# Performance work log

Measured on AMD Instinct MI355X. Metric: run time of the kernel, lower is better.

The kernel has to match this reference:

```python
import jax, jax.numpy as jnp
import numpy as np


def setup_inputs() -> dict:
    key = jax.random.key(0)
    k1, k2, k3 = jax.random.split(key, 3)
    T, B, C, H, W = 8, 4, 128, 96, 96
    h = w = 384  # original visibility-map resolution
    values = jax.random.normal(k1, (T + 1, B, C, H, W), jnp.float32)
    tvmap = jax.random.uniform(k2, (B, 1, h, w), jnp.float32)
    rvmaps = jax.random.uniform(k3, (T, B, 1, h, w), jnp.float32)
    return {"values": values, "tvmap": tvmap, "rvmaps": rvmaps}


def _resize_bin(m, H, W):
    # bilinear resize (half-pixel centers == torch align_corners=False), then > 0.5 threshold
    r = jax.image.resize(m, m.shape[:-2] + (H, W), method="bilinear")
    return (r > 0.5).astype(m.dtype)


def reference(values, tvmap, rvmaps):
    t_feat = values[0]          # [B,C,H,W]
    r_feats = values[1:]        # [T,B,C,H,W]
    T, B, C, H, W = r_feats.shape

    tv = _resize_bin(tvmap, H, W)                           # [B,1,H,W]
    rv = jax.vmap(lambda m: _resize_bin(m, H, W))(rvmaps)   # [T,B,1,H,W]
    vmap_ = tv[None] * rv                                   # [T,B,1,H,W]

    # per-frame masked similarity score gs
    gs = jnp.sum(vmap_ * t_feat[None] * r_feats, axis=(-1, -2, -3))  # [T,B]
    v_sum = jnp.sum(vmap_[:, :, 0], axis=(-1, -2))                   # [T,B]
    empty = v_sum < 1e-4
    gs = jnp.where(empty, 0.0, gs) / (v_sum + empty.astype(gs.dtype)) / C

    gss = gs.transpose(1, 0)[:, None, :, None, None]   # [B,1,T,1,1]
    vmaps = rv.transpose(1, 2, 0, 3, 4)                # [B,1,T,H,W]

    # masked softmax over frame axis (dim=2) with zero-guard
    mv = gss * vmaps
    mx = jnp.max(mv, axis=2, keepdims=True)
    me = jnp.exp(mv - mx) * vmaps
    ms = jnp.sum(me, axis=2, keepdims=True)
    ms = ms + (ms < 1e-4).astype(ms.dtype)
    c_match = jax.lax.stop_gradient(me / ms)           # [B,1,T,H,W]

    rf = r_feats.transpose(1, 2, 0, 3, 4)              # [B,C,T,H,W]
    c_out = jnp.sum(rf * c_match, axis=2)              # [B,C,H,W]

    c_mask = jnp.sum(c_match * vmaps, axis=2)          # [B,1,H,W]
    c_mask = jax.lax.stop_gradient(1.0 - jnp.mean(c_mask, axis=1, keepdims=True))

    out = jnp.concatenate([t_feat, c_out, c_mask], axis=1)  # [B, 2C+1, H, W]
    return out, c_mask, gs
```

## Files before the change

kernel.cpp:

```cpp
#include <hip/hip_runtime.h>
#include <math.h>

#define T_ 8
#define B_ 4
#define C_ 128
#define HW_ 9216
#define IN_HW_ 147456

typedef float nat_f4 __attribute__((ext_vector_type(4)));

__device__ static const double d_wm[8]  = {0.03125, 0.09375, 0.15625, 0.21875,
                                           0.21875, 0.15625, 0.09375, 0.03125};
__device__ static const double d_w0[8]  = {0.0, 0.0, 0.625/3.5, 0.875/3.5,
                                           0.875/3.5, 0.625/3.5, 0.375/3.5, 0.125/3.5};
__device__ static const double d_w95[8] = {0.125/3.5, 0.375/3.5, 0.625/3.5, 0.875/3.5,
                                           0.875/3.5, 0.625/3.5, 0.0, 0.0};

__device__ __forceinline__ float block_sum_256(float v) {
  v += __shfl_xor(v, 1);
  v += __shfl_xor(v, 2);
  v += __shfl_xor(v, 4);
  v += __shfl_xor(v, 8);
  v += __shfl_xor(v, 16);
  v += __shfl_xor(v, 32);
  __shared__ float s[4];
  int lane = threadIdx.x & 63, wv = threadIdx.x >> 6;
  if (lane == 0) s[wv] = v;
  __syncthreads();
  float r = s[0] + s[1] + s[2] + s[3];
  __syncthreads();
  return r;
}

__global__ __launch_bounds__(384) void k_resize(const float* __restrict__ rvmaps,
                                                const float* __restrict__ tvmap,
                                                float* __restrict__ rv,
                                                float* __restrict__ tv) {
  const int job = blockIdx.y;
  const float* img = (job < 32) ? rvmaps + (size_t)job * IN_HW_
                                : tvmap  + (size_t)(job - 32) * IN_HW_;
  float* dst = (job < 32) ? rv + (size_t)job * HW_
                          : tv + (size_t)(job - 32) * HW_;
  const int x  = threadIdx.x % 96;
  const int yg = threadIdx.x / 96;
  const int y0 = blockIdx.x * 16 + yg * 4;

  const double* wys[4];
#pragma unroll
  for (int i = 0; i < 4; ++i) {
    int y = y0 + i;
    wys[i] = (y == 0) ? d_w0 : (y == 95 ? d_w95 : d_wm);
  }

  double acc0 = 0.0, acc1 = 0.0, acc2 = 0.0, acc3 = 0.0;
  const int base = 4 * y0 - 2;
  const int jy_lo = base < 0 ? 0 : base;
  const int jy_hi_raw = 4 * (y0 + 3) + 5;
  const int jy_hi = jy_hi_raw > 383 ? 383 : jy_hi_raw;

  for (int jy = jy_lo; jy <= jy_hi; ++jy) {
    const float* row = img + (size_t)jy * 384;
    double ra;
    if (x == 0) {
      const float4 q0 = *(const float4*)(row);
      const float4 q1 = *(const float4*)(row + 4);
      ra = d_w0[2] * (double)q0.x + d_w0[3] * (double)q0.y +
           d_w0[4] * (double)q0.z + d_w0[5] * (double)q0.w +
           d_w0[6] * (double)q1.x + d_w0[7] * (double)q1.y;
    } else if (x == 95) {
      const float4 q0 = *(const float4*)(row + 376);
      const float4 q1 = *(const float4*)(row + 380);
      ra = d_w95[0] * (double)q0.z + d_w95[1] * (double)q0.w +
           d_w95[2] * (double)q1.x + d_w95[3] * (double)q1.y +
           d_w95[4] * (double)q1.z + d_w95[5] * (double)q1.w;
    } else {
      const int b0 = 4 * x - 4;
      const float4 q0 = *(const float4*)(row + b0);
      const float4 q1 = *(const float4*)(row + b0 + 4);
      const float4 q2 = *(const float4*)(row + b0 + 8);
      ra = d_wm[0] * (double)q0.z + d_wm[1] * (double)q0.w +
           d_wm[2] * (double)q1.x + d_wm[3] * (double)q1.y +
           d_wm[4] * (double)q1.z + d_wm[5] * (double)q1.w +
           d_wm[6] * (double)q2.x + d_wm[7] * (double)q2.y;
    }
    {
      int ky = jy - base;
      if (ky >= 0 && ky < 8) acc0 += wys[0][ky] * ra;
      ky -= 4;
      if (ky >= 0 && ky < 8) acc1 += wys[1][ky] * ra;
      ky -= 4;
      if (ky >= 0 && ky < 8) acc2 += wys[2][ky] * ra;
      ky -= 4;
      if (ky >= 0 && ky < 8) acc3 += wys[3][ky] * ra;
    }
  }
  dst[(size_t)(y0 + 0) * 96 + x] = (acc0 > 0.5) ? 1.0f : 0.0f;
  dst[(size_t)(y0 + 1) * 96 + x] = (acc1 > 0.5) ? 1.0f : 0.0f;
  dst[(size_t)(y0 + 2) * 96 + x] = (acc2 > 0.5) ? 1.0f : 0.0f;
  dst[(size_t)(y0 + 3) * 96 + x] = (acc3 > 0.5) ? 1.0f : 0.0f;
}

__global__ __launch_bounds__(256) void k_gs(const float* __restrict__ values,
                                            const float* __restrict__ rv,
                                            const float* __restrict__ tv,
                                            float* __restrict__ gs_part,
                                            float* __restrict__ out) {
  const int ptile = blockIdx.x;
  const int c     = blockIdx.y;
  const int b     = blockIdx.z;
  const int tid   = threadIdx.x;
  const int p0 = ptile * 1024 + tid * 4;

  const float4 a   = *(const float4*)(values + ((size_t)b * C_ + c) * HW_ + p0);
  const float4 tvv = *(const float4*)(tv + (size_t)b * HW_ + p0);

  {
    nat_f4 an = {a.x, a.y, a.z, a.w};
    __builtin_nontemporal_store(an,
        (nat_f4*)(out + (size_t)b * 257 * HW_ + (size_t)c * HW_ + p0));
  }

  float acc[T_];
#pragma unroll
  for (int t = 0; t < T_; ++t) {
    const float4 rv4 = *(const float4*)(rv + ((size_t)(t * B_ + b)) * HW_ + p0);
    const float4 r = *(const float4*)(values + ((size_t)((1 + t) * B_ + b) * C_ + c) * HW_ + p0);
    const float mx_ = rv4.x * tvv.x, my_ = rv4.y * tvv.y;
    const float mz_ = rv4.z * tvv.z, mw_ = rv4.w * tvv.w;
    acc[t] = mx_ * a.x * r.x + my_ * a.y * r.y + mz_ * a.z * r.z + mw_ * a.w * r.w;
  }

  __shared__ float sred[4][T_];
  const int lane = tid & 63, wv = tid >> 6;
#pragma unroll
  for (int t = 0; t < T_; ++t) {
    float v = acc[t];
    v += __shfl_xor(v, 1);
    v += __shfl_xor(v, 2);
    v += __shfl_xor(v, 4);
    v += __shfl_xor(v, 8);
    v += __shfl_xor(v, 16);
    v += __shfl_xor(v, 32);
    if (lane == 0) sred[wv][t] = v;
  }
  __syncthreads();
  if (tid < T_) {
    const int t = tid;
    const float s = sred[0][t] + sred[1][t] + sred[2][t] + sred[3][t];
    gs_part[(size_t)(t * B_ + b) * (C_ * 9) + c * 9 + ptile] = s;
  }
}

__global__ __launch_bounds__(256) void k_fin(const float* __restrict__ rv,
                                             const float* __restrict__ tv,
                                             const float* __restrict__ gs_part,
                                             float* __restrict__ gsar,
                                             float* __restrict__ out_gs) {
  const int tb = blockIdx.x;
  const int b  = tb % B_;
  const int tid = threadIdx.x;

  const float4* pr = (const float4*)(rv + (size_t)tb * HW_);
  const float4* pt = (const float4*)(tv + (size_t)b  * HW_);
  float vs = 0.f;
  for (int i = tid; i < HW_ / 4; i += 256) {
    const float4 r = pr[i], t = pt[i];
    vs += r.x * t.x + r.y * t.y + r.z * t.z + r.w * t.w;
  }
  vs = block_sum_256(vs);

  const float4* pg = (const float4*)(gs_part + (size_t)tb * (C_ * 9));
  float s = 0.f;
  for (int i = tid; i < (C_ * 9) / 4; i += 256) {
    const float4 v = pg[i];
    s += v.x + v.y + v.z + v.w;
  }
  s = block_sum_256(s);

  if (tid == 0) {
    const bool empty = vs < 1e-4f;
    const float g = (empty ? 0.f : s) / (vs + (empty ? 1.f : 0.f)) / (float)C_;
    gsar[tb] = g;
    out_gs[tb] = g;
  }
}

__global__ __launch_bounds__(256) void k_epi(const float* __restrict__ values,
                                             const float* __restrict__ rv,
                                             const float* __restrict__ gs,
                                             float* __restrict__ out,
                                             float* __restrict__ out_cmask) {
  const int ctile = blockIdx.x;
  const int ptile = blockIdx.y;
  const int b     = blockIdx.z;
  const int tid   = threadIdx.x;
  __shared__ float gsh[T_];
  if (tid < T_) gsh[tid] = gs[tid * B_ + b];
  __syncthreads();

  const int p0 = ptile * 1024 + tid * 4;

  float4 rv4[T_];
#pragma unroll
  for (int t = 0; t < T_; ++t)
    rv4[t] = *(const float4*)(rv + ((size_t)(t * B_ + b)) * HW_ + p0);

  float cm[T_][4];
  float cmask[4];
#pragma unroll
  for (int j = 0; j < 4; ++j) {
    float mv[T_];
    float mx = -1e30f;
#pragma unroll
    for (int t = 0; t < T_; ++t) {
      const float rvv = ((const float*)&rv4[t])[j];
      mv[t] = gsh[t] * rvv;
      mx = fmaxf(mx, mv[t]);
    }
    float e[T_];
    float ms = 0.f;
#pragma unroll
    for (int t = 0; t < T_; ++t) {
      const float rvv = ((const float*)&rv4[t])[j];
      e[t] = expf(mv[t] - mx) * rvv;
      ms += e[t];
    }
    if (ms < 1e-4f) ms += 1.f;
    const float inv = 1.f / ms;
    float cs = 0.f;
#pragma unroll
    for (int t = 0; t < T_; ++t) {
      cm[t][j] = e[t] * inv;
      cs += cm[t][j] * ((const float*)&rv4[t])[j];
    }
    cmask[j] = 1.f - cs;
  }

  const size_t outb = (size_t)b * 257 * HW_;
#pragma unroll 1
  for (int cc = 0; cc < 4; ++cc) {
    const int c = ctile * 4 + cc;
    float4 acc = {0.f, 0.f, 0.f, 0.f};
#pragma unroll
    for (int t = 0; t < T_; ++t) {
      const float4 r = *(const float4*)(values +
          ((size_t)((1 + t) * B_ + b) * C_ + c) * HW_ + p0);
      acc.x += cm[t][0] * r.x;
      acc.y += cm[t][1] * r.y;
      acc.z += cm[t][2] * r.z;
      acc.w += cm[t][3] * r.w;
    }
    nat_f4 accn = {acc.x, acc.y, acc.z, acc.w};
    __builtin_nontemporal_store(accn, (nat_f4*)(out + outb + (size_t)(C_ + c) * HW_ + p0));
  }
  if (ctile == 0) {
    nat_f4 cmv = {cmask[0], cmask[1], cmask[2], cmask[3]};
    __builtin_nontemporal_store(cmv, (nat_f4*)(out + outb + (size_t)256 * HW_ + p0));
    __builtin_nontemporal_store(cmv, (nat_f4*)(out_cmask + (size_t)b * HW_ + p0));
  }
}

extern "C" void kernel_launch(void* const* d_in, const int* in_sizes, int n_in,
                              void* d_out, int out_size, void* d_ws, size_t ws_size,
                              hipStream_t stream) {
  const float* values = (const float*)d_in[0];
  const float* tvmap  = (const float*)d_in[1];
  const float* rvmaps = (const float*)d_in[2];
  float* out = (float*)d_out;

  float* ws      = (float*)d_ws;
  float* rv      = ws;
  float* tv      = rv + (size_t)T_ * B_ * HW_;
  float* gs_part = tv + (size_t)B_ * HW_;
  float* gsar    = gs_part + (size_t)T_ * B_ * C_ * 9;

  float* out_cmask = out + (size_t)B_ * 257 * HW_;
  float* out_gs    = out_cmask + (size_t)B_ * HW_;

  hipLaunchKernelGGL(k_resize, dim3(6, 36),      dim3(384), 0, stream, rvmaps, tvmap, rv, tv);
  hipLaunchKernelGGL(k_gs,     dim3(9, C_, B_),  dim3(256), 0, stream, values, rv, tv, gs_part, out);
  hipLaunchKernelGGL(k_fin,    dim3(32),         dim3(256), 0, stream, rv, tv, gs_part, gsar, out_gs);
  hipLaunchKernelGGL(k_epi,    dim3(32, 9, B_),  dim3(256), 0, stream, values, rv, gsar, out, out_cmask);
}
```

Measured before the change: 322.1 us.

## Fold gs finalization into epilogue kernel and coarsen gs and epilogue blocks

Removes the separate k_fin launch. Each epilogue block now recomputes the visibility sums from rv and tv and reduces the gs partials itself. k_gs blocks each handle three pixel tiles, which cuts the partial count, and epilogue blocks handle 8 channels instead of 4. expf is also swapped for __expf. The cost is that every one of the 576 epilogue blocks redundantly reads all of rv and tv (about 330KB, mostly from L2), which adds a serial prologue before the main work.

```diff
diff --git a/kernel.cpp b/kernel.cpp
--- a/kernel.cpp
+++ b/kernel.cpp
@@ -109,25 +109,28 @@
   const int c     = blockIdx.y;
   const int b     = blockIdx.z;
   const int tid   = threadIdx.x;
-  const int p0 = ptile * 1024 + tid * 4;
-
-  const float4 a   = *(const float4*)(values + ((size_t)b * C_ + c) * HW_ + p0);
-  const float4 tvv = *(const float4*)(tv + (size_t)b * HW_ + p0);
-
-  {
-    nat_f4 an = {a.x, a.y, a.z, a.w};
-    __builtin_nontemporal_store(an,
-        (nat_f4*)(out + (size_t)b * 257 * HW_ + (size_t)c * HW_ + p0));
-  }
 
   float acc[T_];
 #pragma unroll
-  for (int t = 0; t < T_; ++t) {
-    const float4 rv4 = *(const float4*)(rv + ((size_t)(t * B_ + b)) * HW_ + p0);
-    const float4 r = *(const float4*)(values + ((size_t)((1 + t) * B_ + b) * C_ + c) * HW_ + p0);
-    const float mx_ = rv4.x * tvv.x, my_ = rv4.y * tvv.y;
-    const float mz_ = rv4.z * tvv.z, mw_ = rv4.w * tvv.w;
-    acc[t] = mx_ * a.x * r.x + my_ * a.y * r.y + mz_ * a.z * r.z + mw_ * a.w * r.w;
+  for (int t = 0; t < T_; ++t) acc[t] = 0.f;
+
+#pragma unroll
+  for (int i = 0; i < 3; ++i) {
+    const int p0 = ptile * 3072 + i * 1024 + tid * 4;
+    const float4 a   = *(const float4*)(values + ((size_t)b * C_ + c) * HW_ + p0);
+    const float4 tvv = *(const float4*)(tv + (size_t)b * HW_ + p0);
+    {
+      nat_f4 an = {a.x, a.y, a.z, a.w};
+      __builtin_nontemporal_store(an,
+          (nat_f4*)(out + (size_t)b * 257 * HW_ + (size_t)c * HW_ + p0));
+    }
+#pragma unroll
+    for (int t = 0; t < T_; ++t) {
+      const float4 rv4 = *(const float4*)(rv + ((size_t)(t * B_ + b)) * HW_ + p0);
+      const float4 r = *(const float4*)(values + ((size_t)((1 + t) * B_ + b) * C_ + c) * HW_ + p0);
+      acc[t] += (rv4.x * tvv.x) * a.x * r.x + (rv4.y * tvv.y) * a.y * r.y +
+                (rv4.z * tvv.z) * a.z * r.z + (rv4.w * tvv.w) * a.w * r.w;
+    }
   }
 
   __shared__ float sred[4][T_];
@@ -147,56 +150,54 @@
   if (tid < T_) {
     const int t = tid;
     const float s = sred[0][t] + sred[1][t] + sred[2][t] + sred[3][t];
-    gs_part[(size_t)(t * B_ + b) * (C_ * 9) + c * 9 + ptile] = s;
-  }
-}
-
-__global__ __launch_bounds__(256) void k_fin(const float* __restrict__ rv,
+    gs_part[(size_t)(t * B_ + b) * (C_ * 3) + c * 3 + ptile] = s;
+  }
+}
+
+__global__ __launch_bounds__(256) void k_epi(const float* __restrict__ values,
+                                             const float* __restrict__ rv,
                                              const float* __restrict__ tv,
                                              const float* __restrict__ gs_part,
-                                             float* __restrict__ gsar,
+                                             float* __restrict__ out,
+                                             float* __restrict__ out_cmask,
                                              float* __restrict__ out_gs) {
-  const int tb = blockIdx.x;
-  const int b  = tb % B_;
-  const int tid = threadIdx.x;
-
-  const float4* pr = (const float4*)(rv + (size_t)tb * HW_);
-  const float4* pt = (const float4*)(tv + (size_t)b  * HW_);
-  float vs = 0.f;
-  for (int i = tid; i < HW_ / 4; i += 256) {
-    const float4 r = pr[i], t = pt[i];
-    vs += r.x * t.x + r.y * t.y + r.z * t.z + r.w * t.w;
-  }
-  vs = block_sum_256(vs);
-
-  const float4* pg = (const float4*)(gs_part + (size_t)tb * (C_ * 9));
-  float s = 0.f;
-  for (int i = tid; i < (C_ * 9) / 4; i += 256) {
-    const float4 v = pg[i];
-    s += v.x + v.y + v.z + v.w;
-  }
-  s = block_sum_256(s);
-
-  if (tid == 0) {
-    const bool empty = vs < 1e-4f;
-    const float g = (empty ? 0.f : s) / (vs + (empty ? 1.f : 0.f)) / (float)C_;
-    gsar[tb] = g;
-    out_gs[tb] = g;
-  }
-}
-
-__global__ __launch_bounds__(256) void k_epi(const float* __restrict__ values,
-                                             const float* __restrict__ rv,
-                                             const float* __restrict__ gs,
-                                             float* __restrict__ out,
-                                             float* __restrict__ out_cmask) {
   const int ctile = blockIdx.x;
   const int ptile = blockIdx.y;
   const int b     = blockIdx.z;
   const int tid   = threadIdx.x;
+
+  float vsum[T_];
+#pragma unroll
+  for (int t = 0; t < T_; ++t) vsum[t] = 0.f;
+  {
+    const float4* pt = (const float4*)(tv + (size_t)b * HW_);
+    for (int i = tid; i < HW_ / 4; i += 256) {
+      const float4 tvv = pt[i];
+#pragma unroll
+      for (int t = 0; t < T_; ++t) {
+        const float4 r = ((const float4*)(rv + ((size_t)(t * B_ + b)) * HW_))[i];
+        vsum[t] += r.x * tvv.x + r.y * tvv.y + r.z * tvv.z + r.w * tvv.w;
+      }
+    }
+  }
   __shared__ float gsh[T_];
-  if (tid < T_) gsh[tid] = gs[tid * B_ + b];
-  __syncthreads();
+#pragma unroll
+  for (int t = 0; t < T_; ++t) {
+    const float vs = block_sum_256(vsum[t]);
+    float s = 0.f;
+    if (tid < 96) {
+      const float4 v = ((const float4*)(gs_part + (size_t)(t * B_ + b) * (C_ * 3)))[tid];
+      s = v.x + v.y + v.z + v.w;
+    }
+    s = block_sum_256(s);
+    if (tid == 0) {
+      const bool empty = vs < 1e-4f;
+      gsh[t] = (empty ? 0.f : s) / (vs + (empty ? 1.f : 0.f)) / (float)C_;
+    }
+  }
+  __syncthreads();
+  if (ctile == 0 && ptile == 0 && tid < T_)
+    out_gs[tid * B_ + b] = gsh[tid];
 
   const int p0 = ptile * 1024 + tid * 4;
 
@@ -222,7 +223,7 @@
 #pragma unroll
     for (int t = 0; t < T_; ++t) {
       const float rvv = ((const float*)&rv4[t])[j];
-      e[t] = expf(mv[t] - mx) * rvv;
+      e[t] = __expf(mv[t] - mx) * rvv;
       ms += e[t];
     }
     if (ms < 1e-4f) ms += 1.f;
@@ -238,8 +239,8 @@
 
   const size_t outb = (size_t)b * 257 * HW_;
 #pragma unroll 1
-  for (int cc = 0; cc < 4; ++cc) {
-    const int c = ctile * 4 + cc;
+  for (int cc = 0; cc < 8; ++cc) {
+    const int c = ctile * 8 + cc;
     float4 acc = {0.f, 0.f, 0.f, 0.f};
 #pragma unroll
     for (int t = 0; t < T_; ++t) {
@@ -272,13 +273,11 @@
   float* rv      = ws;
   float* tv      = rv + (size_t)T_ * B_ * HW_;
   float* gs_part = tv + (size_t)B_ * HW_;
-  float* gsar    = gs_part + (size_t)T_ * B_ * C_ * 9;
 
   float* out_cmask = out + (size_t)B_ * 257 * HW_;
   float* out_gs    = out_cmask + (size_t)B_ * HW_;
 
   hipLaunchKernelGGL(k_resize, dim3(6, 36),      dim3(384), 0, stream, rvmaps, tvmap, rv, tv);
-  hipLaunchKernelGGL(k_gs,     dim3(9, C_, B_),  dim3(256), 0, stream, values, rv, tv, gs_part, out);
-  hipLaunchKernelGGL(k_fin,    dim3(32),         dim3(256), 0, stream, rv, tv, gs_part, gsar, out_gs);
-  hipLaunchKernelGGL(k_epi,    dim3(32, 9, B_),  dim3(256), 0, stream, values, rv, gsar, out, out_cmask);
-}
+  hipLaunchKernelGGL(k_gs,     dim3(3, C_, B_),  dim3(256), 0, stream, values, rv, tv, gs_part, out);
+  hipLaunchKernelGGL(k_epi,    dim3(16, 9, B_),  dim3(256), 0, stream, values, rv, tv, gs_part, out, out_cmask, out_gs);
+}
```

New measurement: 332.2 us. 3.1% more time.
